# Optimization experiments

Measured on AMD Instinct MI355X. Metric: run time of the kernel, lower is better.

The kernel has to match this reference:

```python
import jax, jax.numpy as jnp
import numpy as np

B, T, D, H = 4, 2048, 1024, 16
HD = D // H  # 64


def setup_inputs() -> dict:
    key = jax.random.key(0)
    ks = jax.random.split(key, 6)
    s = 0.02
    return {
        "embed": jax.random.normal(ks[0], (B, T, D), dtype=jnp.float32),
        "mask": jnp.ones((1, 1, 1, T), dtype=jnp.int32),
        "Wq": jax.random.normal(ks[1], (D, D), dtype=jnp.float32) * s,
        "bq": jnp.zeros((D,), dtype=jnp.float32),
        "Wk": jax.random.normal(ks[2], (D, D), dtype=jnp.float32) * s,
        "bk": jnp.zeros((D,), dtype=jnp.float32),
        "Wv": jax.random.normal(ks[3], (D, D), dtype=jnp.float32) * s,
        "bv": jnp.zeros((D,), dtype=jnp.float32),
        "Wo": jax.random.normal(ks[4], (D, D), dtype=jnp.float32) * s,
        "bo": jnp.zeros((D,), dtype=jnp.float32),
    }


def _attn(embed, Wq, bq, Wk, bk, Wv, bv, Wo, bo, mask):
    b, t, _ = embed.shape
    q = (embed @ Wq + bq).reshape(b, t, H, HD).transpose(0, 2, 1, 3)  # [B,H,T,hd]
    k = (embed @ Wk + bk).reshape(b, t, H, HD).transpose(0, 2, 1, 3)
    v = (embed @ Wv + bv).reshape(b, t, H, HD).transpose(0, 2, 1, 3)
    scores = jnp.einsum("bhqd,bhkd->bhqk", q, k) * (1.0 / np.sqrt(HD))
    scores = jnp.where(mask == 0, jnp.float32(-jnp.inf), scores)
    weights = jax.nn.softmax(scores, axis=-1)  # dropout p=0 in eval
    ctx = jnp.einsum("bhqk,bhkd->bhqd", weights, v)
    merged = ctx.transpose(0, 2, 1, 3).reshape(b, t, D)
    return merged @ Wo + bo


def reference(embed, mask, Wq, bq, Wk, bk, Wv, bv, Wo, bo):
    return _attn(embed, Wq, bq, Wk, bk, Wv, bv, Wo, bo, mask)
```

## Files before the change

kernel.cpp:

```cpp
#include <hip/hip_runtime.h>


typedef __bf16 bf16_t;
typedef bf16_t bf16x8 __attribute__((ext_vector_type(8)));
typedef float  f32x4  __attribute__((ext_vector_type(4)));
typedef unsigned u32x4 __attribute__((ext_vector_type(4)));
typedef unsigned short u16x8 __attribute__((ext_vector_type(8)));
typedef unsigned short u16x4 __attribute__((ext_vector_type(4)));

#define DEV static __device__ __forceinline__

constexpr int Bc = 4, Tc = 2048, Dc = 1024, Hc = 16, HDc = 64;
constexpr int Mc = Bc * Tc;
constexpr int NQKV = 3 * Dc;

DEV unsigned short f2bf(float f) {
  union { float f; unsigned u; } v; v.f = f;
  return (unsigned short)((v.u + 0x7fffu + ((v.u >> 16) & 1u)) >> 16);
}

DEV void gload_lds16(const void* g, const void* ldsbase) {
  unsigned m0v = __builtin_amdgcn_readfirstlane((unsigned)(unsigned long long)ldsbase);
  asm volatile("s_mov_b32 m0, %0\n\t"
               "global_load_lds_dwordx4 %1, off"
               :: "s"(m0v), "v"(g) : "memory");
}

DEV f32x4 mfma16(bf16x8 a, bf16x8 b, f32x4 c) {
  return __builtin_amdgcn_mfma_f32_16x16x32_bf16(a, b, c, 0, 0, 0);
}

DEV void pl32swap(unsigned& a, unsigned& b) {
  asm("v_permlane32_swap_b32 %0, %1" : "+v"(a), "+v"(b));
}
DEV void pl16swap(unsigned& a, unsigned& b) {
  asm("v_permlane16_swap_b32 %0, %1" : "+v"(a), "+v"(b));
}

DEV int fragaddr(int row, int col) {
  return (row >> 4) * 1024 + ((col >> 5) << 9) + (((col >> 3) & 3) << 7)
       + ((row & 15) << 3) + (col & 7);
}

__global__ __launch_bounds__(256) void prep(const float* __restrict__ embed,
                                            const float* __restrict__ Wq,
                                            const float* __restrict__ Wk,
                                            const float* __restrict__ Wv,
                                            const float* __restrict__ Wo,
                                            const float* __restrict__ bq,
                                            const float* __restrict__ bk,
                                            const float* __restrict__ bv,
                                            unsigned short* __restrict__ embed_bf,
                                            unsigned short* __restrict__ WtAll,
                                            float* __restrict__ ball) {
  __shared__ unsigned short tile[64 * 80];
  const int bb = blockIdx.x;
  const int tid = threadIdx.x;

  if (bb < 8192) {
    int i = bb * 256 + tid;
    float4 v = ((const float4*)embed)[i];
    u16x4 o = { f2bf(v.x), f2bf(v.y), f2bf(v.z), f2bf(v.w) };
    *(u16x4*)(embed_bf + (size_t)i * 4) = o;
    return;
  }
  if (bb < 8192 + 1024) {
    int wb = bb - 8192;
    int bx = wb & 15, by = (wb >> 4) & 15, bz = wb >> 8;
    const float* W = bz == 0 ? Wq : bz == 1 ? Wk : bz == 2 ? Wv : Wo;
    unsigned short* dst = WtAll + (size_t)bz * 1024 * 1024;
    const int kb = by * 64, nb = bx * 64;
#pragma unroll
    for (int i = 0; i < 4; i++) {
      int ci = i * 256 + tid;
      int r = ci >> 4, c4 = ci & 15;
      float4 v = *(const float4*)(W + (size_t)(kb + r) * 1024 + nb + c4 * 4);
      u16x4 o = { f2bf(v.x), f2bf(v.y), f2bf(v.z), f2bf(v.w) };
      *(u16x4*)(tile + r * 80 + c4 * 4) = o;
    }
    __syncthreads();
#pragma unroll
    for (int i = 0; i < 2; i++) {
      int ci = i * 256 + tid;
      int n = ci >> 3, c8 = ci & 7;
      u16x8 o;
#pragma unroll
      for (int j = 0; j < 8; j++) o[j] = tile[(c8 * 8 + j) * 80 + n];
      *(u16x8*)(dst + (size_t)(nb + n) * 1024 + kb + c8 * 8) = o;
    }
    return;
  }
#pragma unroll
  for (int it = 0; it < 12; it++) {
    int i = it * 256 + tid;
    ball[i] = (i < 1024) ? bq[i] : (i < 2048) ? bk[i - 1024] : bv[i - 2048];
  }
}

__global__ __launch_bounds__(512, 2) void gemm_qkv8(
    const unsigned short* __restrict__ A,
    const unsigned short* __restrict__ Bt,
    const float* __restrict__ bias,
    unsigned short* __restrict__ Qf,
    unsigned short* __restrict__ Kf,
    unsigned short* __restrict__ Vf) {
  __shared__ unsigned short As_[4 * 8192];
  __shared__ unsigned short Bs_[4 * 8192];

  const int tid = threadIdx.x;
  const int lane = tid & 63, wid = tid >> 6;
  const int lr = lane & 15, lg = lane >> 4;
  const int wr = wid >> 2, wc = wid & 3;

  const int lin = blockIdx.y * 12 + blockIdx.x;
  const int swz = (lin & 7) * 48 + (lin >> 3);
  const int m0 = (swz / 12) * 256, n0 = (swz % 12) * 256;

  size_t gA[2], gB[2];
  int ldsoff[2];
#pragma unroll
  for (int i = 0; i < 2; i++) {
    int ci = i * 512 + tid;
    int row = ci >> 2;
    int cl = (ci & 3) ^ ((row ^ (row >> 2)) & 3);
    gA[i] = (size_t)(m0 + row) * 1024 + cl * 8;
    gB[i] = (size_t)(n0 + row) * 1024 + cl * 8;
    ldsoff[i] = ci * 8;
  }

  int offA[2][4], offB[4];
#pragma unroll
  for (int mq = 0; mq < 2; mq++)
#pragma unroll
    for (int m = 0; m < 4; m++) {
      int row = wr * 128 + mq * 64 + m * 16 + lr;
      offA[mq][m] = row * 32 + ((lg ^ ((row ^ (row >> 2)) & 3)) << 3);
    }
#pragma unroll
  for (int n = 0; n < 4; n++) {
    int row = wc * 64 + n * 16 + lr;
    offB[n] = row * 32 + ((lg ^ ((row ^ (row >> 2)) & 3)) << 3);
  }

  f32x4 acc[8][4] = {};

#define QSTAGE(kt) {                                                         \
    const int sbi_ = (kt) & 3;                                               \
    _Pragma("unroll")                                                        \
    for (int i_ = 0; i_ < 2; i_++) {                                         \
      gload_lds16(A  + gA[i_] + (size_t)(kt) * 32,                           \
                  As_ + sbi_ * 8192 + ldsoff[i_]);                           \
      gload_lds16(Bt + gB[i_] + (size_t)(kt) * 32,                           \
                  Bs_ + sbi_ * 8192 + ldsoff[i_]);                           \
    } }

#define QKTILE(kt, VM, DOST) {                                               \
    const int bi_ = (kt) & 3;                                                \
    const unsigned short* Ab = As_ + bi_ * 8192;                             \
    const unsigned short* Bb = Bs_ + bi_ * 8192;                             \
    asm volatile("s_waitcnt vmcnt(" VM ")" ::: "memory");                    \
    asm volatile("s_barrier" ::: "memory");                                  \
    bf16x8 a0 = *(const bf16x8*)(Ab + offA[0][0]);                           \
    bf16x8 a1 = *(const bf16x8*)(Ab + offA[0][1]);                           \
    bf16x8 a2 = *(const bf16x8*)(Ab + offA[0][2]);                           \
    bf16x8 a3 = *(const bf16x8*)(Ab + offA[0][3]);                           \
    bf16x8 b0 = *(const bf16x8*)(Bb + offB[0]);                              \
    bf16x8 b1 = *(const bf16x8*)(Bb + offB[1]);                              \
    bf16x8 b2 = *(const bf16x8*)(Bb + offB[2]);                              \
    bf16x8 b3 = *(const bf16x8*)(Bb + offB[3]);                              \
    if (DOST) QSTAGE((kt) + 3);                                              \
    __builtin_amdgcn_s_setprio(1);                                           \
    acc[0][0]=mfma16(a0,b0,acc[0][0]); acc[0][1]=mfma16(a0,b1,acc[0][1]);    \
    acc[0][2]=mfma16(a0,b2,acc[0][2]); acc[0][3]=mfma16(a0,b3,acc[0][3]);    \
    acc[1][0]=mfma16(a1,b0,acc[1][0]); acc[1][1]=mfma16(a1,b1,acc[1][1]);    \
    acc[1][2]=mfma16(a1,b2,acc[1][2]); acc[1][3]=mfma16(a1,b3,acc[1][3]);    \
    acc[2][0]=mfma16(a2,b0,acc[2][0]); acc[2][1]=mfma16(a2,b1,acc[2][1]);    \
    acc[2][2]=mfma16(a2,b2,acc[2][2]); acc[2][3]=mfma16(a2,b3,acc[2][3]);    \
    acc[3][0]=mfma16(a3,b0,acc[3][0]); acc[3][1]=mfma16(a3,b1,acc[3][1]);    \
    acc[3][2]=mfma16(a3,b2,acc[3][2]); acc[3][3]=mfma16(a3,b3,acc[3][3]);    \
    __builtin_amdgcn_s_setprio(0);                                           \
    a0 = *(const bf16x8*)(Ab + offA[1][0]);                                  \
    a1 = *(const bf16x8*)(Ab + offA[1][1]);                                  \
    a2 = *(const bf16x8*)(Ab + offA[1][2]);                                  \
    a3 = *(const bf16x8*)(Ab + offA[1][3]);                                  \
    __builtin_amdgcn_s_setprio(1);                                           \
    acc[4][0]=mfma16(a0,b0,acc[4][0]); acc[4][1]=mfma16(a0,b1,acc[4][1]);    \
    acc[4][2]=mfma16(a0,b2,acc[4][2]); acc[4][3]=mfma16(a0,b3,acc[4][3]);    \
    acc[5][0]=mfma16(a1,b0,acc[5][0]); acc[5][1]=mfma16(a1,b1,acc[5][1]);    \
    acc[5][2]=mfma16(a1,b2,acc[5][2]); acc[5][3]=mfma16(a1,b3,acc[5][3]);    \
    acc[6][0]=mfma16(a2,b0,acc[6][0]); acc[6][1]=mfma16(a2,b1,acc[6][1]);    \
    acc[6][2]=mfma16(a2,b2,acc[6][2]); acc[6][3]=mfma16(a2,b3,acc[6][3]);    \
    acc[7][0]=mfma16(a3,b0,acc[7][0]); acc[7][1]=mfma16(a3,b1,acc[7][1]);    \
    acc[7][2]=mfma16(a3,b2,acc[7][2]); acc[7][3]=mfma16(a3,b3,acc[7][3]);    \
    __builtin_amdgcn_s_setprio(0); }

  QSTAGE(0); QSTAGE(1); QSTAGE(2);

#pragma unroll 1
  for (int kt = 0; kt < 29; ++kt) {
    QKTILE(kt, "8", 1);
  }
  QKTILE(29, "8", 0);
  QKTILE(30, "4", 0);
  QKTILE(31, "0", 0);
#undef QSTAGE
#undef QKTILE

#pragma unroll
  for (int mq = 0; mq < 8; mq++)
#pragma unroll
    for (int n = 0; n < 4; n++)
#pragma unroll
      for (int r = 0; r < 4; r++) {
        int row = m0 + wr * 128 + (mq >> 2) * 64 + (mq & 3) * 16 + lg * 4 + r;
        int col = n0 + wc * 64 + n * 16 + lr;
        float v = acc[mq][n][r] + bias[col];
        int bb = row >> 11, tl = row & 2047;
        if (col < Dc) {
          v *= 0.18033688f;
          int h = col >> 6, d = col & 63;
          Qf[(size_t)(bb * 16 + h) * 131072 + fragaddr(tl, d)] = f2bf(v);
        } else if (col < 2 * Dc) {
          int c = col - Dc, h = c >> 6, d = c & 63;
          Kf[(size_t)(bb * 16 + h) * 131072 + fragaddr(tl, d)] = f2bf(v);
        } else {
          int c = col - 2 * Dc, h = c >> 6, d = c & 63;
          Vf[(size_t)(bb * 16 + h) * 131072 + (tl >> 6) * 4096 + fragaddr(d, tl & 63)] = f2bf(v);
        }
      }
}

__global__ __launch_bounds__(256) void gemm_bt(const unsigned short* __restrict__ A,
                                               const unsigned short* __restrict__ Bt,
                                               const float* __restrict__ bias,
                                               float* __restrict__ Cout,
                                               int N, int K) {
  __shared__ unsigned short As[128 * 64];
  __shared__ unsigned short Bs[128 * 64];
  const int tid = threadIdx.x;
  const int lane = tid & 63, wid = tid >> 6;
  const int lr = lane & 15, lg = lane >> 4;
  const int wrow = wid >> 1, wcol = wid & 1;
  const int m0 = blockIdx.y * 128, n0 = blockIdx.x * 128;

  f32x4 acc[4][4] = {};

  for (int k0 = 0; k0 < K; k0 += 64) {
#pragma unroll
    for (int i = 0; i < 4; i++) {
      int ci = i * 256 + tid;
      int row = ci >> 3, ph = ci & 7;
      int cl = ph ^ (row & 7);
      gload_lds16(A + (size_t)(m0 + row) * K + k0 + cl * 8, As + (size_t)(i * 256 + wid * 64) * 8);
      gload_lds16(Bt + (size_t)(n0 + row) * K + k0 + cl * 8, Bs + (size_t)(i * 256 + wid * 64) * 8);
    }
    asm volatile("s_waitcnt vmcnt(0)" ::: "memory");
    __syncthreads();
#pragma unroll
    for (int kk = 0; kk < 2; kk++) {
      bf16x8 av[4], bv[4];
#pragma unroll
      for (int m = 0; m < 4; m++) {
        int row = wrow * 64 + m * 16 + lr;
        int ph = (kk * 4 + lg) ^ (row & 7);
        av[m] = *(const bf16x8*)(As + row * 64 + ph * 8);
      }
#pragma unroll
      for (int n = 0; n < 4; n++) {
        int row = wcol * 64 + n * 16 + lr;
        int ph = (kk * 4 + lg) ^ (row & 7);
        bv[n] = *(const bf16x8*)(Bs + row * 64 + ph * 8);
      }
#pragma unroll
      for (int m = 0; m < 4; m++)
#pragma unroll
        for (int n = 0; n < 4; n++)
          acc[m][n] = mfma16(av[m], bv[n], acc[m][n]);
    }
    __syncthreads();
  }

#pragma unroll
  for (int m = 0; m < 4; m++)
#pragma unroll
    for (int n = 0; n < 4; n++)
#pragma unroll
      for (int r = 0; r < 4; r++) {
        int row = m0 + wrow * 64 + m * 16 + lg * 4 + r;
        int col = n0 + wcol * 64 + n * 16 + lr;
        Cout[(size_t)row * N + col] = acc[m][n][r] + bias[col];
      }
}

__global__ __launch_bounds__(256, 2) void flash7(const unsigned short* __restrict__ Qf,
                                                 const unsigned short* __restrict__ Kf,
                                                 const unsigned short* __restrict__ Vf,
                                                 const int* __restrict__ mask,
                                                 unsigned short* __restrict__ merged) {
  const int tid = threadIdx.x;
  const int lane = tid & 63, wid = tid >> 6;
  const int lr = lane & 15, lg = lane >> 4;

  const int lin = blockIdx.y * 8 + blockIdx.x;
  const int swz = (lin & 7) * 64 + (lin >> 3);
  const int qb = swz & 7, bh = swz >> 3;
  const int b = bh >> 4, h = bh & 15;
  const int wq = qb * 256 + wid * 64;

  const unsigned short* Qb = Qf + (size_t)bh * 131072;
  const unsigned short* Kb = Kf + (size_t)bh * 131072;
  const unsigned short* Vb = Vf + (size_t)bh * 131072;

  bf16x8 qf[4][2];
#pragma unroll
  for (int qn = 0; qn < 4; qn++)
#pragma unroll
    for (int kk = 0; kk < 2; kk++)
      qf[qn][kk] = *(const bf16x8*)(Qb + ((wq >> 4) + qn) * 1024 + kk * 512 + lane * 8);

  f32x4 o[4][4] = {};
  f32x4 lacc[4] = {};

  bf16x8 ones;
#pragma unroll
  for (int j = 0; j < 8; j++) ones[j] = (bf16_t)1.0f;

  bool allone = true;
#pragma unroll
  for (int j = 0; j < 8; j++) {
    int4 mv = ((const int4*)mask)[j * 64 + lane];
    allone = allone && (mv.x != 0) && (mv.y != 0) && (mv.z != 0) && (mv.w != 0);
  }
  const bool nomask = (__ballot(allone) == ~0ull);

#pragma unroll 2
  for (int tile = 0; tile < 32; tile++) {
    bf16x8 kf[4][2];
#pragma unroll
    for (int n = 0; n < 4; n++)
#pragma unroll
      for (int kk = 0; kk < 2; kk++)
        kf[n][kk] = *(const bf16x8*)(Kb + (tile * 4 + n) * 1024 + kk * 512 + lane * 8);
    bf16x8 vf[4][2];
#pragma unroll
    for (int dn = 0; dn < 4; dn++)
#pragma unroll
      for (int kk = 0; kk < 2; kk++)
        vf[dn][kk] = *(const bf16x8*)(Vb + tile * 4096 + dn * 1024 + kk * 512 + lane * 8);

    unsigned long long mb = ~0ull;
    if (!nomask) mb = __ballot(mask[tile * 64 + lane] != 0);

    unsigned pk[4][4][2];
#pragma unroll
    for (int kvn = 0; kvn < 4; kvn++) {
      f32x4 st[4] = {};
#pragma unroll
      for (int qn = 0; qn < 4; qn++) {
        st[qn] = mfma16(kf[kvn][0], qf[qn][0], st[qn]);
        st[qn] = mfma16(kf[kvn][1], qf[qn][1], st[qn]);
      }
      if (mb != ~0ull) {
#pragma unroll
        for (int r = 0; r < 4; r++)
          if (!((mb >> (kvn * 16 + lg * 4 + r)) & 1ull)) {
#pragma unroll
            for (int qn = 0; qn < 4; qn++) st[qn][r] = -1e30f;
          }
      }
#pragma unroll
      for (int qn = 0; qn < 4; qn++) {
        float e[4];
#pragma unroll
        for (int r = 0; r < 4; r++)
          asm("v_exp_f32 %0, %1" : "=v"(e[r]) : "v"(st[qn][r]));
        asm("v_cvt_pk_bf16_f32 %0, %1, %2" : "=v"(pk[qn][kvn][0]) : "v"(e[0]), "v"(e[1]));
        asm("v_cvt_pk_bf16_f32 %0, %1, %2" : "=v"(pk[qn][kvn][1]) : "v"(e[2]), "v"(e[3]));
      }
    }

    bf16x8 pa[4][2];
#pragma unroll
    for (int qn = 0; qn < 4; qn++)
#pragma unroll
      for (int m = 0; m < 2; m++) {
        unsigned a0 = pk[qn][2 * m][0], b0 = pk[qn][2 * m + 1][0];
        unsigned a1 = pk[qn][2 * m][1], b1 = pk[qn][2 * m + 1][1];
        pl32swap(a0, b0);
        pl32swap(a1, b1);
        pl16swap(a0, b0);
        pl16swap(a1, b1);
        u32x4 w = { a0, a1, b0, b1 };
        pa[qn][m] = __builtin_bit_cast(bf16x8, w);
      }

    __builtin_amdgcn_s_setprio(1);
#pragma unroll
    for (int qn = 0; qn < 4; qn++) {
#pragma unroll
      for (int dn = 0; dn < 4; dn++) {
        o[qn][dn] = mfma16(pa[qn][0], vf[dn][0], o[qn][dn]);
        o[qn][dn] = mfma16(pa[qn][1], vf[dn][1], o[qn][dn]);
      }
      lacc[qn] = mfma16(pa[qn][0], ones, lacc[qn]);
      lacc[qn] = mfma16(pa[qn][1], ones, lacc[qn]);
    }
    __builtin_amdgcn_s_setprio(0);
  }

#pragma unroll
  for (int qn = 0; qn < 4; qn++)
#pragma unroll
    for (int r = 0; r < 4; r++) {
      float inv = 1.0f / lacc[qn][r];
      int grow = b * Tc + wq + qn * 16 + lg * 4 + r;
#pragma unroll
      for (int dn = 0; dn < 4; dn++) {
        int gcol = h * HDc + dn * 16 + lr;
        merged[(size_t)grow * Dc + gcol] = f2bf(o[qn][dn][r] * inv);
      }
    }
}

extern "C" void kernel_launch(void* const* d_in, const int* in_sizes, int n_in,
                              void* d_out, int out_size, void* d_ws, size_t ws_size,
                              hipStream_t stream) {
  const float* embed = (const float*)d_in[0];
  const int*   mask  = (const int*)d_in[1];
  const float* Wq = (const float*)d_in[2];
  const float* bq = (const float*)d_in[3];
  const float* Wk = (const float*)d_in[4];
  const float* bk = (const float*)d_in[5];
  const float* Wv = (const float*)d_in[6];
  const float* bv = (const float*)d_in[7];
  const float* Wo = (const float*)d_in[8];
  const float* bo = (const float*)d_in[9];
  float* out = (float*)d_out;

  char* ws = (char*)d_ws;
  unsigned short* embed_bf = (unsigned short*)ws; ws += (size_t)Mc * Dc * 2;
  unsigned short* WtAll    = (unsigned short*)ws; ws += (size_t)4 * Dc * Dc * 2;
  float*          ball     = (float*)ws;          ws += 16384;
  unsigned short* Qf       = (unsigned short*)ws; ws += (size_t)Mc * Dc * 2;
  unsigned short* Kf       = (unsigned short*)ws; ws += (size_t)Mc * Dc * 2;
  unsigned short* Vf       = (unsigned short*)ws; ws += (size_t)Mc * Dc * 2;
  unsigned short* merged   = (unsigned short*)ws; ws += (size_t)Mc * Dc * 2;

  prep<<<8192 + 1024 + 1, 256, 0, stream>>>(embed, Wq, Wk, Wv, Wo, bq, bk, bv,
                                            embed_bf, WtAll, ball);
  gemm_qkv8<<<dim3(12, 32), 512, 0, stream>>>(embed_bf, WtAll, ball, Qf, Kf, Vf);
  flash7<<<dim3(8, 64), 256, 0, stream>>>(Qf, Kf, Vf, mask, merged);
  gemm_bt<<<dim3(8, 64), 256, 0, stream>>>(merged, WtAll + (size_t)3 * Dc * Dc, bo, out, Dc, Dc);
}
```

Measured before the change: 192.6 us.

## Compute transposed QKV GEMM and pack Q/K epilogue into vectorized fragment stores

The QKV projection now computes the transposed product, with weights as the M operand and embeddings as the N operand, so each lane's accumulator registers run along the feature dimension. For Q and K tiles the epilogue loads bias as float4, converts pairs with packed bf16 conversion, and shuffles lanes (pl32swap/pl16swap) so each lane writes 16-byte vector stores in fragment layout. This replaces many scattered 2-byte stores. V keeps a scalar scattered store path. The swizzled grid mapping is swapped, which changes L2 reuse patterns.

```diff
diff --git a/kernel.cpp b/kernel.cpp
--- a/kernel.cpp
+++ b/kernel.cpp
@@ -97,9 +97,9 @@
   }
 }
 
-__global__ __launch_bounds__(512, 2) void gemm_qkv8(
-    const unsigned short* __restrict__ A,
-    const unsigned short* __restrict__ Bt,
+__global__ __launch_bounds__(512, 2) void gemm_qkv11(
+    const unsigned short* __restrict__ Wt,
+    const unsigned short* __restrict__ Eb,
     const float* __restrict__ bias,
     unsigned short* __restrict__ Qf,
     unsigned short* __restrict__ Kf,
@@ -114,7 +114,7 @@
 
   const int lin = blockIdx.y * 12 + blockIdx.x;
   const int swz = (lin & 7) * 48 + (lin >> 3);
-  const int m0 = (swz / 12) * 256, n0 = (swz % 12) * 256;
+  const int m0 = (swz % 12) * 256, n0 = (swz / 12) * 256;
 
   size_t gA[2], gB[2];
   int ldsoff[2];
@@ -148,9 +148,9 @@
     const int sbi_ = (kt) & 3;                                               \
     _Pragma("unroll")                                                        \
     for (int i_ = 0; i_ < 2; i_++) {                                         \
-      gload_lds16(A  + gA[i_] + (size_t)(kt) * 32,                           \
+      gload_lds16(Wt + gA[i_] + (size_t)(kt) * 32,                           \
                   As_ + sbi_ * 8192 + ldsoff[i_]);                           \
-      gload_lds16(Bt + gB[i_] + (size_t)(kt) * 32,                           \
+      gload_lds16(Eb + gB[i_] + (size_t)(kt) * 32,                           \
                   Bs_ + sbi_ * 8192 + ldsoff[i_]);                           \
     } }
 
@@ -206,28 +206,67 @@
 #undef QSTAGE
 #undef QKTILE
 
-#pragma unroll
-  for (int mq = 0; mq < 8; mq++)
-#pragma unroll
-    for (int n = 0; n < 4; n++)
-#pragma unroll
-      for (int r = 0; r < 4; r++) {
-        int row = m0 + wr * 128 + (mq >> 2) * 64 + (mq & 3) * 16 + lg * 4 + r;
-        int col = n0 + wc * 64 + n * 16 + lr;
-        float v = acc[mq][n][r] + bias[col];
-        int bb = row >> 11, tl = row & 2047;
-        if (col < Dc) {
-          v *= 0.18033688f;
-          int h = col >> 6, d = col & 63;
-          Qf[(size_t)(bb * 16 + h) * 131072 + fragaddr(tl, d)] = f2bf(v);
-        } else if (col < 2 * Dc) {
-          int c = col - Dc, h = c >> 6, d = c & 63;
-          Kf[(size_t)(bb * 16 + h) * 131072 + fragaddr(tl, d)] = f2bf(v);
-        } else {
-          int c = col - 2 * Dc, h = c >> 6, d = c & 63;
-          Vf[(size_t)(bb * 16 + h) * 131072 + (tl >> 6) * 4096 + fragaddr(d, tl & 63)] = f2bf(v);
+  const int ft = m0 >> 8;
+  if (ft < 8) {
+#pragma unroll
+    for (int g = 0; g < 2; g++) {
+      const int fb = m0 + wr * 128 + g * 64;
+      const bool isQ = (fb < Dc);
+      unsigned short* const dstm = isQ ? Qf : Kf;
+      const int head = (isQ ? fb : fb - Dc) >> 6;
+      float4 b4[4];
+#pragma unroll
+      for (int mq = 0; mq < 4; mq++)
+        b4[mq] = *(const float4*)(bias + fb + mq * 16 + lg * 4);
+#pragma unroll
+      for (int n = 0; n < 4; n++) {
+        unsigned w8[4][2];
+#pragma unroll
+        for (int mq = 0; mq < 4; mq++) {
+          float e0 = acc[g * 4 + mq][n][0] + b4[mq].x;
+          float e1 = acc[g * 4 + mq][n][1] + b4[mq].y;
+          float e2 = acc[g * 4 + mq][n][2] + b4[mq].z;
+          float e3 = acc[g * 4 + mq][n][3] + b4[mq].w;
+          if (isQ) {
+            e0 *= 0.18033688f; e1 *= 0.18033688f;
+            e2 *= 0.18033688f; e3 *= 0.18033688f;
+          }
+          asm("v_cvt_pk_bf16_f32 %0, %1, %2" : "=v"(w8[mq][0]) : "v"(e0), "v"(e1));
+          asm("v_cvt_pk_bf16_f32 %0, %1, %2" : "=v"(w8[mq][1]) : "v"(e2), "v"(e3));
         }
-      }
+        const int t = n0 + wc * 64 + n * 16;
+        const int bb = t >> 11, tl = t & 2047;
+        unsigned short* dst = dstm + (size_t)(bb * 16 + head) * 131072
+                            + (tl >> 4) * 1024;
+#pragma unroll
+        for (int half = 0; half < 2; half++) {
+          unsigned a0 = w8[2 * half][0], c0 = w8[2 * half + 1][0];
+          unsigned a1 = w8[2 * half][1], c1 = w8[2 * half + 1][1];
+          pl32swap(a0, c0);
+          pl32swap(a1, c1);
+          pl16swap(a0, c0);
+          pl16swap(a1, c1);
+          u32x4 w = { a0, a1, c0, c1 };
+          *(u32x4*)(dst + half * 512 + lane * 8) = w;
+        }
+      }
+    }
+  } else {
+#pragma unroll
+    for (int m = 0; m < 8; m++)
+#pragma unroll
+      for (int n = 0; n < 4; n++)
+#pragma unroll
+        for (int r = 0; r < 4; r++) {
+          int f = m0 + wr * 128 + m * 16 + lg * 4 + r;
+          int t = n0 + wc * 64 + n * 16 + lr;
+          float v = acc[m][n][r] + bias[f];
+          int c = f - 2 * Dc, head = c >> 6, d = c & 63;
+          int bb = t >> 11, tl = t & 2047;
+          Vf[(size_t)(bb * 16 + head) * 131072 + (tl >> 6) * 4096
+             + fragaddr(d, tl & 63)] = f2bf(v);
+        }
+  }
 }
 
 __global__ __launch_bounds__(256) void gemm_bt(const unsigned short* __restrict__ A,
@@ -448,7 +487,7 @@
 
   prep<<<8192 + 1024 + 1, 256, 0, stream>>>(embed, Wq, Wk, Wv, Wo, bq, bk, bv,
                                             embed_bf, WtAll, ball);
-  gemm_qkv8<<<dim3(12, 32), 512, 0, stream>>>(embed_bf, WtAll, ball, Qf, Kf, Vf);
+  gemm_qkv11<<<dim3(12, 32), 512, 0, stream>>>(WtAll, embed_bf, ball, Qf, Kf, Vf);
   flash7<<<dim3(8, 64), 256, 0, stream>>>(Qf, Kf, Vf, mask, merged);
   gemm_bt<<<dim3(8, 64), 256, 0, stream>>>(merged, WtAll + (size_t)3 * Dc * Dc, bo, out, Dc, Dc);
 }
```

New measurement: 177.6 us. -7.8%, faster.
